# Kernel optimization log

Measured on AMD Instinct MI355X. Metric: run time of the kernel, lower is better.

The kernel has to match this reference:

```python
import jax, jax.numpy as jnp
import numpy as np

B, SQ, SK, D, UNITS = 4, 2048, 2048, 1024, 1024

def setup_inputs() -> dict:
    key = jax.random.key(0)
    ks = jax.random.split(key, 5)
    scale = 1.0 / np.sqrt(D)
    return {
        "q": jax.random.normal(ks[0], (B, SQ, D), dtype=jnp.float32),
        "k": jax.random.normal(ks[1], (B, SK, D), dtype=jnp.float32),
        "v": jax.random.normal(ks[2], (B, SK, D), dtype=jnp.float32),
        "W1_w": jax.random.normal(ks[3], (D, UNITS), dtype=jnp.float32) * scale,
        "W1_b": jnp.zeros((UNITS,), dtype=jnp.float32),
        "W2_w": jax.random.normal(ks[4], (D, UNITS), dtype=jnp.float32) * scale,
        "W2_b": jnp.zeros((UNITS,), dtype=jnp.float32),
    }

def reference(q, k, v, W1_w, W1_b, W2_w, W2_b):
    # Dense projections (keras Dense: x @ W + b)
    l1 = q @ W1_w + W1_b            # [B, Sq, units]
    l2 = k @ W2_w + W2_b            # [B, Sk, units]
    # score = l1 @ l2^T, scaled by sqrt(score.shape[2]) == sqrt(Sk) (as in original)
    inv_scale = 1.0 / np.sqrt(k.shape[1]).astype(np.float32)
    score = jnp.einsum('bqu,bku->bqk', l1, l2) * inv_scale  # [B, Sq, Sk]
    dist = jax.nn.softmax(score, axis=-1)
    att = jnp.einsum('bqk,bkd->bqd', dist, v)               # [B, Sq, d_v]
    return att
```

## Files before the change

### kernel.cpp

```cpp
#include <hip/hip_runtime.h>
#include <cmath>
#include <stdint.h>


typedef short short8 __attribute__((ext_vector_type(8)));
typedef float f32x4 __attribute__((ext_vector_type(4)));
typedef __bf16 bf16x8 __attribute__((ext_vector_type(8)));

typedef __attribute__((address_space(3))) void lds_void;
typedef __attribute__((address_space(1))) void gbl_void;

__device__ __forceinline__ unsigned short f2b(float x) {
    unsigned u = __builtin_bit_cast(unsigned, x);
    u += 0x7fffu + ((u >> 16) & 1u);
    return (unsigned short)(u >> 16);
}

__global__ void prep_kernel(const float* __restrict__ q,
                            const float* __restrict__ k,
                            const float* __restrict__ v,
                            const float* __restrict__ W1,
                            const float* __restrict__ W2,
                            unsigned short* __restrict__ qbf,
                            unsigned short* __restrict__ kbf,
                            unsigned short* __restrict__ vT,
                            unsigned short* __restrict__ W1t,
                            unsigned short* __restrict__ W2t) {
    __shared__ float tile[32][33];
    const int bz = blockIdx.z;
    const int t = threadIdx.x;

    if (bz >= 6) {
        const float* in = (bz < 8) ? q : k;
        unsigned short* out = (bz < 8) ? qbf : kbf;
        const long zi = (bz - 6) & 1;
        const long fb = zi * 2048 + blockIdx.y * 64 + blockIdx.x;
        const long i = (fb * 256 + t) * 8;
        float4 a = *(const float4*)(in + i);
        float4 b = *(const float4*)(in + i + 4);
        union { short8 v8; unsigned short u[8]; } r;
        r.u[0] = f2b(a.x); r.u[1] = f2b(a.y); r.u[2] = f2b(a.z); r.u[3] = f2b(a.w);
        r.u[4] = f2b(b.x); r.u[5] = f2b(b.y); r.u[6] = f2b(b.z); r.u[7] = f2b(b.w);
        *(short8*)(out + i) = r.v8;
        return;
    }

    const float* in;
    unsigned short* out;
    int R, C;
    if (bz < 4) {
        R = 2048; C = 1024;
        in = v + (long)bz * R * C;
        out = vT + (long)bz * R * C;
    } else {
        R = 1024; C = 1024;
        if (blockIdx.x >= 32) return;
        in = (bz == 4) ? W1 : W2;
        out = (bz == 4) ? W1t : W2t;
    }
    const int rt = blockIdx.x * 32, ct = blockIdx.y * 32;
    {
        int r = t >> 3, c4 = (t & 7) * 4;
        float4 a = *(const float4*)(in + (long)(rt + r) * C + ct + c4);
        tile[r][c4 + 0] = a.x; tile[r][c4 + 1] = a.y;
        tile[r][c4 + 2] = a.z; tile[r][c4 + 3] = a.w;
    }
    __syncthreads();
    {
        int c = t >> 3, rg = (t & 7) * 4;
        ushort4 o;
        o.x = f2b(tile[rg + 0][c]); o.y = f2b(tile[rg + 1][c]);
        o.z = f2b(tile[rg + 2][c]); o.w = f2b(tile[rg + 3][c]);
        *(ushort4*)(out + (long)(ct + c) * R + rt + rg) = o;
    }
}

__device__ __forceinline__ void load16_to_lds(const unsigned short* g,
                                              unsigned short* l) {
    __builtin_amdgcn_global_load_lds((gbl_void*)g, (lds_void*)l, 16, 0, 0);
}

template <int MODE>
__global__ void gemm_bt_kernel(const unsigned short* __restrict__ A,
                               const unsigned short* __restrict__ Bt,
                               const float* __restrict__ bias0,
                               const float* __restrict__ bias1,
                               float* __restrict__ rowsum,
                               void* __restrict__ Cout,
                               int M, int N, int K,
                               float scale,
                               long sA, long sB, long sC) {
    __shared__ __align__(16) unsigned short As[128 * 64];
    __shared__ __align__(16) unsigned short Bs[128 * 64];

    int bx, by, bz;
    {
        const int nx = gridDim.x;
        const int Rt = gridDim.y * gridDim.z;
        if ((Rt & 7) == 0) {
            int flat = ((int)blockIdx.z * gridDim.y + blockIdx.y) * nx + blockIdx.x;
            int rpx = Rt >> 3;
            int c = flat & 7;
            int j = flat >> 3;
            bx = j / rpx;
            int yg = c * rpx + (j - bx * rpx);
            bz = yg / gridDim.y;
            by = yg - bz * gridDim.y;
        } else {
            bx = blockIdx.x; by = blockIdx.y; bz = blockIdx.z;
        }
    }

    A  += (long)bz * sA;
    Bt += (long)bz * sB;

    const int t = threadIdx.x;
    const int lane = t & 63;
    const int wave = t >> 6;
    const int wm = wave >> 1, wn = wave & 1;
    const int row0 = by * 128;
    const int col0 = bx * 128;

    const int rS = lane >> 3;
    const int kOffS = ((lane & 7) ^ rS) * 8;
    const unsigned short* gA[4];
    const unsigned short* gB[4];
    unsigned short* lA[4];
    unsigned short* lB[4];
#pragma unroll
    for (int i = 0; i < 4; i++) {
        const int rowl = i * 32 + wave * 8 + rS;
        const int ldsrow = i * 32 + wave * 8;
        gA[i] = A  + (long)(row0 + rowl) * K + kOffS;
        gB[i] = Bt + (long)(col0 + rowl) * K + kOffS;
        lA[i] = As + ldsrow * 64;
        lB[i] = Bs + ldsrow * 64;
    }

    const int lr = lane & 15;
    const int quad = lane >> 4;
    const int pc0 = (quad ^ (lr & 7)) * 8;
    const int pc1 = ((4 + quad) ^ (lr & 7)) * 8;

    f32x4 acc[4][4];
#pragma unroll
    for (int i = 0; i < 4; i++)
#pragma unroll
        for (int j = 0; j < 4; j++) acc[i][j] = f32x4{0.f, 0.f, 0.f, 0.f};

    for (int k0 = 0; k0 < K; k0 += 64) {
#pragma unroll
        for (int i = 0; i < 4; i++) {
            load16_to_lds(gA[i] + k0, lA[i]);
            load16_to_lds(gB[i] + k0, lB[i]);
        }
        __syncthreads();

#pragma unroll
        for (int ks = 0; ks < 2; ks++) {
            const int pc = ks ? pc1 : pc0;
            bf16x8 a[4], b[4];
#pragma unroll
            for (int i = 0; i < 4; i++) {
                a[i] = __builtin_bit_cast(bf16x8,
                    *(const short8*)(As + (wm * 64 + i * 16 + lr) * 64 + pc));
                b[i] = __builtin_bit_cast(bf16x8,
                    *(const short8*)(Bs + (wn * 64 + i * 16 + lr) * 64 + pc));
            }
#pragma unroll
            for (int i = 0; i < 4; i++)
#pragma unroll
                for (int j = 0; j < 4; j++)
                    acc[i][j] = __builtin_amdgcn_mfma_f32_16x16x32_bf16(
                        a[i], b[j], acc[i][j], 0, 0, 0);
        }
        __syncthreads();
    }

    const long cbase = (long)bz * sC;

    if (MODE == 0) {
        const float* bp = (bz && bias1) ? bias1 : bias0;
#pragma unroll
        for (int j = 0; j < 4; j++) {
            const int gcol = col0 + wn * 64 + j * 16 + lr;
            const float bv = bp[gcol];
#pragma unroll
            for (int i = 0; i < 4; i++) {
                const int growb = row0 + wm * 64 + i * 16 + quad * 4;
#pragma unroll
                for (int r = 0; r < 4; r++) {
                    float val = acc[i][j][r] * scale + bv;
                    ((unsigned short*)Cout)[cbase + (long)(growb + r) * N + gcol] = f2b(val);
                }
            }
        }
    } else if (MODE == 1) {
        float psum[4][4];
#pragma unroll
        for (int i = 0; i < 4; i++)
#pragma unroll
            for (int r = 0; r < 4; r++) psum[i][r] = 0.f;
#pragma unroll
        for (int j = 0; j < 4; j++) {
            const int gcol = col0 + wn * 64 + j * 16 + lr;
#pragma unroll
            for (int i = 0; i < 4; i++) {
                const int growb = row0 + wm * 64 + i * 16 + quad * 4;
#pragma unroll
                for (int r = 0; r < 4; r++) {
                    float e = __expf(acc[i][j][r] * scale);
                    psum[i][r] += e;
                    ((unsigned short*)Cout)[cbase + (long)(growb + r) * N + gcol] = f2b(e);
                }
            }
        }
#pragma unroll
        for (int i = 0; i < 4; i++)
#pragma unroll
            for (int r = 0; r < 4; r++) {
                float s = psum[i][r];
                s += __shfl_xor(s, 1);
                s += __shfl_xor(s, 2);
                s += __shfl_xor(s, 4);
                s += __shfl_xor(s, 8);
                if (lr == 0) {
                    const int grow = row0 + wm * 64 + i * 16 + quad * 4 + r;
                    atomicAdd(rowsum + (long)bz * M + grow, s);
                }
            }
    } else {
#pragma unroll
        for (int i = 0; i < 4; i++) {
            const int growb = row0 + wm * 64 + i * 16 + quad * 4;
#pragma unroll
            for (int r = 0; r < 4; r++) {
                const float inv = 1.0f / rowsum[(long)bz * M + growb + r];
#pragma unroll
                for (int j = 0; j < 4; j++) {
                    const int gcol = col0 + wn * 64 + j * 16 + lr;
                    ((float*)Cout)[cbase + (long)(growb + r) * N + gcol] =
                        acc[i][j][r] * inv;
                }
            }
        }
    }
}

extern "C" void kernel_launch(void* const* d_in, const int* in_sizes, int n_in,
                              void* d_out, int out_size, void* d_ws, size_t ws_size,
                              hipStream_t stream) {
    const float* q   = (const float*)d_in[0];
    const float* k   = (const float*)d_in[1];
    const float* v   = (const float*)d_in[2];
    const float* W1w = (const float*)d_in[3];
    const float* W1b = (const float*)d_in[4];
    const float* W2w = (const float*)d_in[5];
    const float* W2b = (const float*)d_in[6];
    float* out = (float*)d_out;

    const int B = 4, SQ = 2048, SK = 2048, D = 1024, U = 1024;
    char* ws = (char*)d_ws;
    const size_t MB = 1024 * 1024;
    unsigned short* qbf = (unsigned short*)(ws + 0);
    unsigned short* kbf = (unsigned short*)(ws + 16 * MB);
    unsigned short* vT  = (unsigned short*)(ws + 32 * MB);
    unsigned short* W1t = (unsigned short*)(ws + 48 * MB);
    unsigned short* W2t = (unsigned short*)(ws + 50 * MB);
    unsigned short* l1  = (unsigned short*)(ws + 52 * MB);
    unsigned short* l2  = (unsigned short*)(ws + 68 * MB);
    unsigned short* sc  = (unsigned short*)(ws + 0);
    float* rowsum = (float*)(ws + 50 * MB);

    prep_kernel<<<dim3(64, 32, 10), 256, 0, stream>>>(
        q, k, v, W1w, W2w, qbf, kbf, vT, W1t, W2t);
    gemm_bt_kernel<0><<<dim3(U / 128, (B * SQ) / 128, 2), 256, 0, stream>>>(
        qbf, W1t, W1b, W2b, nullptr, l1, B * SQ, U, D, 1.0f,
        (long)8 * 1024 * 1024, (long)1024 * 1024, (long)8 * 1024 * 1024);
    hipMemsetAsync(rowsum, 0, (size_t)B * SQ * sizeof(float), stream);
    const float invs = 1.0f / sqrtf((float)SK);
    gemm_bt_kernel<1><<<dim3(SK / 128, SQ / 128, B), 256, 0, stream>>>(
        l1, l2, nullptr, nullptr, rowsum, sc, SQ, SK, U, invs,
        (long)SQ * U, (long)SK * U, (long)SQ * SK);
    gemm_bt_kernel<2><<<dim3(D / 128, SQ / 128, B), 256, 0, stream>>>(
        sc, vT, nullptr, nullptr, rowsum, out, SQ, D, SK, 1.0f,
        (long)SQ * SK, (long)D * SK, (long)SQ * D);
}
```

Baseline: 268.0 us.

## Reassociate projections into a fused W1·W2ᵀ product and drop the key projection

The score is rewritten as q·(W1·W2ᵀ)·kᵀ plus a per-key bias term b1·W2ᵀ·kᵀ. Bias terms that are constant per query row are dropped because softmax ignores them. A small 1024×1024 weight product is built inside the prep kernel, which removes the full key-projection GEMM over all batches. The rowsum atomics and memset are replaced by per-tile partial sums that the attention kernel reduces and inverts in LDS. The score buffers are packed into freed workspace regions. The cost is an extra weight GEMM and a GEMV, plus bf16 rounding of the fused weight matrix, which changes the numerical error profile.

```diff
diff --git a/kernel.cpp b/kernel.cpp
--- a/kernel.cpp
+++ b/kernel.cpp
@@ -15,104 +15,66 @@
     u += 0x7fffu + ((u >> 16) & 1u);
     return (unsigned short)(u >> 16);
 }
-
-__global__ void prep_kernel(const float* __restrict__ q,
-                            const float* __restrict__ k,
-                            const float* __restrict__ v,
-                            const float* __restrict__ W1,
-                            const float* __restrict__ W2,
-                            unsigned short* __restrict__ qbf,
-                            unsigned short* __restrict__ kbf,
-                            unsigned short* __restrict__ vT,
-                            unsigned short* __restrict__ W1t,
-                            unsigned short* __restrict__ W2t) {
-    __shared__ float tile[32][33];
-    const int bz = blockIdx.z;
-    const int t = threadIdx.x;
-
-    if (bz >= 6) {
-        const float* in = (bz < 8) ? q : k;
-        unsigned short* out = (bz < 8) ? qbf : kbf;
-        const long zi = (bz - 6) & 1;
-        const long fb = zi * 2048 + blockIdx.y * 64 + blockIdx.x;
-        const long i = (fb * 256 + t) * 8;
-        float4 a = *(const float4*)(in + i);
-        float4 b = *(const float4*)(in + i + 4);
-        union { short8 v8; unsigned short u[8]; } r;
-        r.u[0] = f2b(a.x); r.u[1] = f2b(a.y); r.u[2] = f2b(a.z); r.u[3] = f2b(a.w);
-        r.u[4] = f2b(b.x); r.u[5] = f2b(b.y); r.u[6] = f2b(b.z); r.u[7] = f2b(b.w);
-        *(short8*)(out + i) = r.v8;
-        return;
-    }
-
-    const float* in;
-    unsigned short* out;
-    int R, C;
-    if (bz < 4) {
-        R = 2048; C = 1024;
-        in = v + (long)bz * R * C;
-        out = vT + (long)bz * R * C;
-    } else {
-        R = 1024; C = 1024;
-        if (blockIdx.x >= 32) return;
-        in = (bz == 4) ? W1 : W2;
-        out = (bz == 4) ? W1t : W2t;
-    }
-    const int rt = blockIdx.x * 32, ct = blockIdx.y * 32;
-    {
-        int r = t >> 3, c4 = (t & 7) * 4;
-        float4 a = *(const float4*)(in + (long)(rt + r) * C + ct + c4);
-        tile[r][c4 + 0] = a.x; tile[r][c4 + 1] = a.y;
-        tile[r][c4 + 2] = a.z; tile[r][c4 + 3] = a.w;
-    }
-    __syncthreads();
-    {
-        int c = t >> 3, rg = (t & 7) * 4;
-        ushort4 o;
-        o.x = f2b(tile[rg + 0][c]); o.y = f2b(tile[rg + 1][c]);
-        o.z = f2b(tile[rg + 2][c]); o.w = f2b(tile[rg + 3][c]);
-        *(ushort4*)(out + (long)(ct + c) * R + rt + rg) = o;
-    }
-}
+__device__ __forceinline__ float b2f(unsigned short x) {
+    unsigned u = ((unsigned)x) << 16;
+    return __builtin_bit_cast(float, u);
+}
+
+struct Off4 { long o[4]; };
 
 __device__ __forceinline__ void load16_to_lds(const unsigned short* g,
                                               unsigned short* l) {
     __builtin_amdgcn_global_load_lds((gbl_void*)g, (lds_void*)l, 16, 0, 0);
 }
 
+__device__ __forceinline__ void mfma_tile(const unsigned short* As,
+                                          const unsigned short* Bs,
+                                          int wm, int wn, int lr, int quad,
+                                          f32x4 acc[4][4]) {
+    const int pc0 = (quad ^ (lr & 7)) * 8;
+    const int pc1 = ((4 + quad) ^ (lr & 7)) * 8;
+#pragma unroll
+    for (int ks = 0; ks < 2; ks++) {
+        const int pc = ks ? pc1 : pc0;
+        bf16x8 a[4], b[4];
+#pragma unroll
+        for (int i = 0; i < 4; i++) {
+            a[i] = __builtin_bit_cast(bf16x8,
+                *(const short8*)(As + (wm * 64 + i * 16 + lr) * 64 + pc));
+            b[i] = __builtin_bit_cast(bf16x8,
+                *(const short8*)(Bs + (wn * 64 + i * 16 + lr) * 64 + pc));
+        }
+#pragma unroll
+        for (int i = 0; i < 4; i++)
+#pragma unroll
+            for (int j = 0; j < 4; j++)
+                acc[i][j] = __builtin_amdgcn_mfma_f32_16x16x32_bf16(
+                    a[i], b[j], acc[i][j], 0, 0, 0);
+    }
+}
+
 template <int MODE>
-__global__ void gemm_bt_kernel(const unsigned short* __restrict__ A,
-                               const unsigned short* __restrict__ Bt,
-                               const float* __restrict__ bias0,
-                               const float* __restrict__ bias1,
-                               float* __restrict__ rowsum,
-                               void* __restrict__ Cout,
-                               int M, int N, int K,
-                               float scale,
-                               long sA, long sB, long sC) {
-    __shared__ __align__(16) unsigned short As[128 * 64];
-    __shared__ __align__(16) unsigned short Bs[128 * 64];
-
+__device__ __forceinline__ void gemm_core(
+        int flat, int nx, int ny, int nz,
+        const unsigned short* __restrict__ A0, Off4 aoff,
+        const unsigned short* __restrict__ Bt0, long sB,
+        const float* __restrict__ vv, float* __restrict__ partial,
+        void* __restrict__ C0, Off4 coff,
+        int N, int K, float scale,
+        unsigned short* As, unsigned short* Bs) {
     int bx, by, bz;
     {
-        const int nx = gridDim.x;
-        const int Rt = gridDim.y * gridDim.z;
-        if ((Rt & 7) == 0) {
-            int flat = ((int)blockIdx.z * gridDim.y + blockIdx.y) * nx + blockIdx.x;
-            int rpx = Rt >> 3;
-            int c = flat & 7;
-            int j = flat >> 3;
-            bx = j / rpx;
-            int yg = c * rpx + (j - bx * rpx);
-            bz = yg / gridDim.y;
-            by = yg - bz * gridDim.y;
-        } else {
-            bx = blockIdx.x; by = blockIdx.y; bz = blockIdx.z;
-        }
-    }
-
-    A  += (long)bz * sA;
-    Bt += (long)bz * sB;
+        const int Rt = ny * nz;
+        int rpx = Rt >> 3;
+        int c = flat & 7;
+        int j = flat >> 3;
+        bx = j / rpx;
+        int yg = c * rpx + (j - bx * rpx);
+        bz = yg / ny;
+        by = yg - bz * ny;
+    }
+    const unsigned short* A  = A0  + aoff.o[bz];
+    const unsigned short* Bt = Bt0 + (long)bz * sB;
 
     const int t = threadIdx.x;
     const int lane = t & 63;
@@ -139,8 +101,6 @@
 
     const int lr = lane & 15;
     const int quad = lane >> 4;
-    const int pc0 = (quad ^ (lr & 7)) * 8;
-    const int pc1 = ((4 + quad) ^ (lr & 7)) * 8;
 
     f32x4 acc[4][4];
 #pragma unroll
@@ -155,44 +115,23 @@
             load16_to_lds(gB[i] + k0, lB[i]);
         }
         __syncthreads();
-
-#pragma unroll
-        for (int ks = 0; ks < 2; ks++) {
-            const int pc = ks ? pc1 : pc0;
-            bf16x8 a[4], b[4];
-#pragma unroll
-            for (int i = 0; i < 4; i++) {
-                a[i] = __builtin_bit_cast(bf16x8,
-                    *(const short8*)(As + (wm * 64 + i * 16 + lr) * 64 + pc));
-                b[i] = __builtin_bit_cast(bf16x8,
-                    *(const short8*)(Bs + (wn * 64 + i * 16 + lr) * 64 + pc));
-            }
-#pragma unroll
-            for (int i = 0; i < 4; i++)
-#pragma unroll
-                for (int j = 0; j < 4; j++)
-                    acc[i][j] = __builtin_amdgcn_mfma_f32_16x16x32_bf16(
-                        a[i], b[j], acc[i][j], 0, 0, 0);
-        }
+        mfma_tile(As, Bs, wm, wn, lr, quad, acc);
         __syncthreads();
     }
 
-    const long cbase = (long)bz * sC;
+    const long cbase = coff.o[bz];
 
     if (MODE == 0) {
-        const float* bp = (bz && bias1) ? bias1 : bias0;
 #pragma unroll
         for (int j = 0; j < 4; j++) {
             const int gcol = col0 + wn * 64 + j * 16 + lr;
-            const float bv = bp[gcol];
 #pragma unroll
             for (int i = 0; i < 4; i++) {
                 const int growb = row0 + wm * 64 + i * 16 + quad * 4;
 #pragma unroll
-                for (int r = 0; r < 4; r++) {
-                    float val = acc[i][j][r] * scale + bv;
-                    ((unsigned short*)Cout)[cbase + (long)(growb + r) * N + gcol] = f2b(val);
-                }
+                for (int r = 0; r < 4; r++)
+                    ((unsigned short*)C0)[cbase + (long)(growb + r) * N + gcol] =
+                        f2b(acc[i][j][r]);
             }
         }
     } else if (MODE == 1) {
@@ -204,14 +143,15 @@
 #pragma unroll
         for (int j = 0; j < 4; j++) {
             const int gcol = col0 + wn * 64 + j * 16 + lr;
+            const float vvv = vv[(long)bz * 2048 + gcol];
 #pragma unroll
             for (int i = 0; i < 4; i++) {
                 const int growb = row0 + wm * 64 + i * 16 + quad * 4;
 #pragma unroll
                 for (int r = 0; r < 4; r++) {
-                    float e = __expf(acc[i][j][r] * scale);
+                    float e = __expf((acc[i][j][r] + vvv) * scale);
                     psum[i][r] += e;
-                    ((unsigned short*)Cout)[cbase + (long)(growb + r) * N + gcol] = f2b(e);
+                    ((unsigned short*)C0)[cbase + (long)(growb + r) * N + gcol] = f2b(e);
                 }
             }
         }
@@ -226,25 +166,223 @@
                 s += __shfl_xor(s, 8);
                 if (lr == 0) {
                     const int grow = row0 + wm * 64 + i * 16 + quad * 4 + r;
-                    atomicAdd(rowsum + (long)bz * M + grow, s);
+                    partial[((long)bz * 2048 + grow) * 32 + bx * 2 + wn] = s;
                 }
             }
     } else {
+        float* rowinv = (float*)(void*)As;
+        if (t < 128) {
+            const float* pr = partial + ((long)bz * 2048 + row0 + t) * 32;
+            float s = 0.f;
+#pragma unroll
+            for (int c4 = 0; c4 < 32; c4 += 4) {
+                float4 v4 = *(const float4*)(pr + c4);
+                s += v4.x + v4.y + v4.z + v4.w;
+            }
+            rowinv[t] = 1.0f / s;
+        }
+        __syncthreads();
 #pragma unroll
         for (int i = 0; i < 4; i++) {
-            const int growb = row0 + wm * 64 + i * 16 + quad * 4;
+            const int lrow = wm * 64 + i * 16 + quad * 4;
 #pragma unroll
             for (int r = 0; r < 4; r++) {
-                const float inv = 1.0f / rowsum[(long)bz * M + growb + r];
+                const float inv = rowinv[lrow + r];
 #pragma unroll
                 for (int j = 0; j < 4; j++) {
                     const int gcol = col0 + wn * 64 + j * 16 + lr;
-                    ((float*)Cout)[cbase + (long)(growb + r) * N + gcol] =
+                    ((float*)C0)[cbase + (long)(row0 + lrow + r) * N + gcol] =
                         acc[i][j][r] * inv;
                 }
             }
         }
     }
+}
+
+__global__ void prep_kernel(const float* __restrict__ q,
+                            const float* __restrict__ k,
+                            const float* __restrict__ v,
+                            const float* __restrict__ W1,
+                            const float* __restrict__ W2,
+                            const float* __restrict__ b1,
+                            unsigned short* __restrict__ qbf,
+                            unsigned short* __restrict__ kbf,
+                            unsigned short* __restrict__ vT,
+                            unsigned short* __restrict__ Mt,
+                            float* __restrict__ w2b1) {
+    __shared__ __align__(16) unsigned short As[128 * 64];
+    __shared__ __align__(16) unsigned short Bs[128 * 64];
+    const int flat = blockIdx.x;
+    const int t = threadIdx.x;
+
+    if (flat < 64) {
+        const int by = flat >> 3, bx = flat & 7;
+        const int row0 = by * 128, col0 = bx * 128;
+        const int lane = t & 63, wave = t >> 6;
+        const int wm = wave >> 1, wn = wave & 1;
+        const int lr = lane & 15, quad = lane >> 4;
+        const int srow = t >> 1;
+        const int hk = (t & 1) * 32;
+        const float* gA = W2 + (long)(row0 + srow) * 1024 + hk;
+        const float* gB = W1 + (long)(col0 + srow) * 1024 + hk;
+        unsigned short* lA = As + srow * 64;
+        unsigned short* lB = Bs + srow * 64;
+        const int xr = srow & 7;
+
+        f32x4 acc[4][4];
+#pragma unroll
+        for (int i = 0; i < 4; i++)
+#pragma unroll
+            for (int j = 0; j < 4; j++) acc[i][j] = f32x4{0.f, 0.f, 0.f, 0.f};
+
+        for (int k0 = 0; k0 < 1024; k0 += 64) {
+#pragma unroll
+            for (int m2 = 0; m2 < 2; m2++) {
+                const float* src = m2 ? gB : gA;
+                unsigned short* dst = m2 ? lB : lA;
+#pragma unroll
+                for (int ci = 0; ci < 4; ci++) {
+                    float4 f0 = *(const float4*)(src + k0 + ci * 8);
+                    float4 f1 = *(const float4*)(src + k0 + ci * 8 + 4);
+                    union { short8 v8; unsigned short u[8]; } r;
+                    r.u[0] = f2b(f0.x); r.u[1] = f2b(f0.y);
+                    r.u[2] = f2b(f0.z); r.u[3] = f2b(f0.w);
+                    r.u[4] = f2b(f1.x); r.u[5] = f2b(f1.y);
+                    r.u[6] = f2b(f1.z); r.u[7] = f2b(f1.w);
+                    const int phys = ((hk >> 3) + ci) ^ xr;
+                    *(short8*)(dst + phys * 8) = r.v8;
+                }
+            }
+            __syncthreads();
+            mfma_tile(As, Bs, wm, wn, lr, quad, acc);
+            __syncthreads();
+        }
+#pragma unroll
+        for (int j = 0; j < 4; j++) {
+            const int gcol = col0 + wn * 64 + j * 16 + lr;
+#pragma unroll
+            for (int i = 0; i < 4; i++) {
+                const int growb = row0 + wm * 64 + i * 16 + quad * 4;
+#pragma unroll
+                for (int r = 0; r < 4; r++)
+                    Mt[(long)(growb + r) * 1024 + gcol] = f2b(acc[i][j][r]);
+            }
+        }
+        return;
+    }
+    if (flat < 96) {
+        const int b = flat - 64;
+        const int row = b * 32 + (t >> 3);
+        const int oct = t & 7;
+        const float* wr = W2 + (long)row * 1024 + oct * 128;
+        const float* br = b1 + oct * 128;
+        float s = 0.f;
+#pragma unroll
+        for (int i = 0; i < 32; i++) {
+            float4 w = *(const float4*)(wr + i * 4);
+            float4 bb = *(const float4*)(br + i * 4);
+            s += w.x * bb.x + w.y * bb.y + w.z * bb.z + w.w * bb.w;
+        }
+        s += __shfl_xor(s, 1);
+        s += __shfl_xor(s, 2);
+        s += __shfl_xor(s, 4);
+        if (oct == 0) w2b1[row] = s;
+        return;
+    }
+    const int u = flat - 96;
+    if (u < 8192) {
+        float (*tile)[33] = (float (*)[33])(void*)As;
+        const int vz = u >> 11;
+        const int rem = u & 2047;
+        const int vy = rem >> 6, vx = rem & 63;
+        const float* in = v + (long)vz * 2048 * 1024;
+        unsigned short* outp = vT + (long)vz * 1024 * 2048;
+        const int rt = vx * 32, ct = vy * 32;
+        {
+            int r = t >> 3, c4 = (t & 7) * 4;
+            float4 a = *(const float4*)(in + (long)(rt + r) * 1024 + ct + c4);
+            tile[r][c4 + 0] = a.x; tile[r][c4 + 1] = a.y;
+            tile[r][c4 + 2] = a.z; tile[r][c4 + 3] = a.w;
+        }
+        __syncthreads();
+        {
+            int c = t >> 3, rg = (t & 7) * 4;
+            ushort4 o;
+            o.x = f2b(tile[rg + 0][c]); o.y = f2b(tile[rg + 1][c]);
+            o.z = f2b(tile[rg + 2][c]); o.w = f2b(tile[rg + 3][c]);
+            *(ushort4*)(outp + (long)(ct + c) * 2048 + rt + rg) = o;
+        }
+        return;
+    }
+    const int c = u - 8192;
+    const float* in = (c < 4096) ? q : k;
+    unsigned short* outp = (c < 4096) ? qbf : kbf;
+    const long i = (((long)(c & 4095)) * 256 + t) * 8;
+    float4 a = *(const float4*)(in + i);
+    float4 b = *(const float4*)(in + i + 4);
+    union { short8 v8; unsigned short uu[8]; } r;
+    r.uu[0] = f2b(a.x); r.uu[1] = f2b(a.y); r.uu[2] = f2b(a.z); r.uu[3] = f2b(a.w);
+    r.uu[4] = f2b(b.x); r.uu[5] = f2b(b.y); r.uu[6] = f2b(b.z); r.uu[7] = f2b(b.w);
+    *(short8*)(outp + i) = r.v8;
+}
+
+__global__ void tq_kernel(const unsigned short* __restrict__ qbf,
+                          const unsigned short* __restrict__ Mt,
+                          const unsigned short* __restrict__ kbf,
+                          const float* __restrict__ w2b1,
+                          unsigned short* __restrict__ tq,
+                          float* __restrict__ vv) {
+    __shared__ __align__(16) unsigned short As[128 * 64];
+    __shared__ __align__(16) unsigned short Bs[128 * 64];
+    const int flat = blockIdx.x;
+    if (flat < 512) {
+        Off4 z = {{0, 0, 0, 0}};
+        gemm_core<0>(flat, 8, 64, 1, qbf, z, Mt, 0, nullptr, nullptr,
+                     tq, z, 1024, 1024, 1.0f, As, Bs);
+        return;
+    }
+    const int t = threadIdx.x;
+    const int row = (flat - 512) * 128 + (t >> 1);
+    const int half = t & 1;
+    const unsigned short* kr = kbf + (long)row * 1024 + half * 512;
+    const float* wvp = w2b1 + half * 512;
+    float s = 0.f;
+#pragma unroll 8
+    for (int i = 0; i < 64; i++) {
+        union { short8 v8; unsigned short u[8]; } r;
+        r.v8 = *(const short8*)(kr + i * 8);
+#pragma unroll
+        for (int e = 0; e < 8; e++) s += b2f(r.u[e]) * wvp[i * 8 + e];
+    }
+    s += __shfl_xor(s, 1);
+    if (half == 0) vv[row] = s;
+}
+
+__global__ void score_kernel(const unsigned short* __restrict__ tq,
+                             const unsigned short* __restrict__ kbf,
+                             const float* __restrict__ vv,
+                             float* __restrict__ partial,
+                             unsigned short* __restrict__ scbase,
+                             Off4 scoff) {
+    __shared__ __align__(16) unsigned short As[128 * 64];
+    __shared__ __align__(16) unsigned short Bs[128 * 64];
+    const long S = 2048L * 1024;
+    Off4 aoff = {{0, S, 2 * S, 3 * S}};
+    gemm_core<1>(blockIdx.x, 16, 16, 4, tq, aoff, kbf, S, vv, partial,
+                 scbase, scoff, 2048, 1024, 0.02209708691207961f, As, Bs);
+}
+
+__global__ void att_kernel(const unsigned short* __restrict__ scbase,
+                           Off4 scoff,
+                           const unsigned short* __restrict__ vT,
+                           float* __restrict__ partial,
+                           float* __restrict__ out) {
+    __shared__ __align__(16) unsigned short As[128 * 64];
+    __shared__ __align__(16) unsigned short Bs[128 * 64];
+    const long S = 2048L * 1024;
+    Off4 coff = {{0, S, 2 * S, 3 * S}};
+    gemm_core<2>(blockIdx.x, 8, 16, 4, scbase, scoff, vT, S, nullptr, partial,
+                 out, coff, 1024, 2048, 1.0f, As, Bs);
 }
 
 extern "C" void kernel_launch(void* const* d_in, const int* in_sizes, int n_in,
@@ -257,32 +395,25 @@
     const float* W1b = (const float*)d_in[4];
     const float* W2w = (const float*)d_in[5];
     const float* W2b = (const float*)d_in[6];
+    (void)W2b;
     float* out = (float*)d_out;
 
-    const int B = 4, SQ = 2048, SK = 2048, D = 1024, U = 1024;
     char* ws = (char*)d_ws;
     const size_t MB = 1024 * 1024;
-    unsigned short* qbf = (unsigned short*)(ws + 0);
-    unsigned short* kbf = (unsigned short*)(ws + 16 * MB);
-    unsigned short* vT  = (unsigned short*)(ws + 32 * MB);
-    unsigned short* W1t = (unsigned short*)(ws + 48 * MB);
-    unsigned short* W2t = (unsigned short*)(ws + 50 * MB);
-    unsigned short* l1  = (unsigned short*)(ws + 52 * MB);
-    unsigned short* l2  = (unsigned short*)(ws + 68 * MB);
-    unsigned short* sc  = (unsigned short*)(ws + 0);
-    float* rowsum = (float*)(ws + 50 * MB);
-
-    prep_kernel<<<dim3(64, 32, 10), 256, 0, stream>>>(
-        q, k, v, W1w, W2w, qbf, kbf, vT, W1t, W2t);
-    gemm_bt_kernel<0><<<dim3(U / 128, (B * SQ) / 128, 2), 256, 0, stream>>>(
-        qbf, W1t, W1b, W2b, nullptr, l1, B * SQ, U, D, 1.0f,
-        (long)8 * 1024 * 1024, (long)1024 * 1024, (long)8 * 1024 * 1024);
-    hipMemsetAsync(rowsum, 0, (size_t)B * SQ * sizeof(float), stream);
-    const float invs = 1.0f / sqrtf((float)SK);
-    gemm_bt_kernel<1><<<dim3(SK / 128, SQ / 128, B), 256, 0, stream>>>(
-        l1, l2, nullptr, nullptr, rowsum, sc, SQ, SK, U, invs,
-        (long)SQ * U, (long)SK * U, (long)SQ * SK);
-    gemm_bt_kernel<2><<<dim3(D / 128, SQ / 128, B), 256, 0, stream>>>(
-        sc, vT, nullptr, nullptr, rowsum, out, SQ, D, SK, 1.0f,
-        (long)SQ * SK, (long)D * SK, (long)SQ * D);
-}
+    unsigned short* qbf  = (unsigned short*)(ws + 0);
+    unsigned short* kbf  = (unsigned short*)(ws + 16 * MB);
+    unsigned short* vT   = (unsigned short*)(ws + 32 * MB);
+    float* partial       = (float*)(ws + 48 * MB);
+    float* vv            = (float*)(ws + 49 * MB);
+    float* w2b1          = (float*)(ws + 50 * MB);
+    unsigned short* Mt   = (unsigned short*)(ws + 52 * MB);
+    unsigned short* tq   = (unsigned short*)(ws + 68 * MB);
+    unsigned short* scb  = (unsigned short*)ws;
+    Off4 scoff = {{0, 4L * 1024 * 1024, 26L * 1024 * 1024, 30L * 1024 * 1024}};
+
+    prep_kernel<<<16480, 256, 0, stream>>>(q, k, v, W1w, W2w, W1b,
+                                           qbf, kbf, vT, Mt, w2b1);
+    tq_kernel<<<576, 256, 0, stream>>>(qbf, Mt, kbf, w2b1, tq, vv);
+    score_kernel<<<1024, 256, 0, stream>>>(tq, kbf, vv, partial, scb, scoff);
+    att_kernel<<<512, 256, 0, stream>>>(scb, scoff, vT, partial, out);
+}
```

Result: slower. 400.0 us (+49.2%).
